# Kernel tuning notes

Hardware: AMD Instinct MI355X
Metric: run time of the kernel (lower is better)

The kernel has to match this reference:

```python
import jax, jax.numpy as jnp
import numpy as np

N_NODES = 100000
N_EDGES = 1600000
IN_CH, HID, OUT_CH = 512, 16, 64


def setup_inputs() -> dict:
    key = jax.random.key(0)
    ks = jax.random.split(key, 9)
    x = jax.random.normal(ks[0], (N_NODES, IN_CH), dtype=jnp.float32)
    edge_index1 = jax.random.randint(ks[1], (2, N_EDGES), 0, N_NODES, dtype=jnp.int32)
    edge_weight1 = jax.random.uniform(ks[2], (N_EDGES,), dtype=jnp.float32)
    edge_index2 = jax.random.randint(ks[3], (2, N_EDGES), 0, N_NODES, dtype=jnp.int32)
    edge_weight2 = jax.random.uniform(ks[4], (N_EDGES,), dtype=jnp.float32)
    W1 = jax.random.normal(ks[5], (IN_CH, HID), dtype=jnp.float32) / np.sqrt(IN_CH)
    b1 = jnp.zeros((HID,), dtype=jnp.float32)
    W2 = jax.random.normal(ks[6], (HID, OUT_CH), dtype=jnp.float32) / np.sqrt(HID)
    b2 = jnp.zeros((OUT_CH,), dtype=jnp.float32)
    return dict(x=x, edge_index1=edge_index1, edge_weight1=edge_weight1,
                edge_index2=edge_index2, edge_weight2=edge_weight2,
                W1=W1, b1=b1, W2=W2, b2=b2, num_nodes=N_NODES)


def _gcn_conv(x, W, b, row, col, w, num_nodes):
    # symmetric-normalized GCN aggregation: out = D^-1/2 A D^-1/2 (x W) + b
    deg = jax.ops.segment_sum(w, row, num_segments=num_nodes)  # [N]
    dinv = jnp.where(deg > 0, jax.lax.rsqrt(jnp.maximum(deg, 1e-12)), 0.0)
    norm = dinv[row] * w * dinv[col]                            # [E]
    h = x @ W                                                   # [N, F_out]
    msg = norm[:, None] * h[col]                                # [E, F_out]
    return jax.ops.segment_sum(msg, row, num_segments=num_nodes) + b


def reference(x, edge_index1, edge_weight1, edge_index2, edge_weight2,
              W1, b1, W2, b2, num_nodes):
    # concat edge lists; torch_sparse.coalesce(op='add') merges duplicates by
    # summing weights — the subsequent degree + scatter-add aggregation is
    # invariant to that dedup, so we run directly on the concatenated list.
    ei = jnp.concatenate([edge_index1, edge_index2], axis=1)    # [2, 2E]
    ew = jnp.concatenate([edge_weight1, edge_weight2])          # [2E]
    row, col = ei[0], ei[1]
    h = _gcn_conv(x, W1, b1, row, col, ew, num_nodes)
    h = jax.nn.relu(h)  # dropout is identity in eval mode
    h = _gcn_conv(h, W2, b2, row, col, ew, num_nodes)
    return jax.nn.log_softmax(h, axis=1)
```

## Files before the change

kernel.cpp:

```cpp
#include <hip/hip_runtime.h>
#include <hip/hip_bf16.h>

#define IN_CH 512
#define HID 16
#define OUT_CH 64
#define CAP 20480

typedef __attribute__((ext_vector_type(8))) short bf16x8;
typedef __attribute__((ext_vector_type(4))) float f32x4;

__device__ inline unsigned short f2bf(float f) {
    unsigned int u = __float_as_uint(f);
    return (unsigned short)((u + 0x7fffu + ((u >> 16) & 1u)) >> 16);
}

union A8 { bf16x8 v; short2 p[4]; };
__device__ inline short2 pk2(float a, float b) {
    union { __hip_bfloat162 h; short2 s; } u;
    u.h = __float22bfloat162_rn(make_float2(a, b));
    return u.s;
}

__global__ void k_init(int* __restrict__ cursors, int nbk) {
    int i = threadIdx.x;
    if (i < nbk) cursors[i] = i * CAP;
}

__global__ __launch_bounds__(1024) void k_partition(const int* __restrict__ ei1, const float* __restrict__ w1, int E1,
                                                    const int* __restrict__ ei2, const float* __restrict__ w2, int E2,
                                                    int* __restrict__ cursors,
                                                    uint2* __restrict__ packed, int Et) {
    __shared__ int hist[256];
    __shared__ int cur[256];
    int tid = threadIdx.x;
    if (tid < 256) hist[tid] = 0;
    __syncthreads();
    int e0 = blockIdx.x * 16384 + tid;
    #pragma unroll
    for (int j = 0; j < 16; ++j) {
        int e = e0 + j * 1024;
        if (e < Et) {
            int r = (e < E1) ? ei1[e] : ei2[e - E1];
            atomicAdd(&hist[r >> 9], 1);
        }
    }
    __syncthreads();
    if (tid < 256) {
        int h = hist[tid];
        cur[tid] = (h > 0) ? atomicAdd(&cursors[tid], h) : 0;
    }
    __syncthreads();
    #pragma unroll
    for (int j = 0; j < 16; ++j) {
        int e = e0 + j * 1024;
        if (e < Et) {
            int r, c; float w;
            if (e < E1) { r = ei1[e]; c = ei1[e + E1]; w = w1[e]; }
            else        { int f = e - E1; r = ei2[f]; c = ei2[f + E2]; w = w2[f]; }
            int b = r >> 9;
            int pos = atomicAdd(&cur[b], 1);
            packed[pos] = make_uint2(((unsigned)(r & 511) << 17) | (unsigned)c,
                                     __float_as_uint(w));
        }
    }
}

__global__ void k_bucket_scan(const int* __restrict__ cursors, int* __restrict__ cbase, int nbk) {
    __shared__ int s[256];
    int tid = threadIdx.x;
    int v = (tid < nbk) ? (cursors[tid] - tid * CAP) : 0;
    s[tid] = v;
    __syncthreads();
    for (int off = 1; off < 256; off <<= 1) {
        int t = (tid >= off) ? s[tid - off] : 0;
        __syncthreads();
        s[tid] += t;
        __syncthreads();
    }
    if (tid < nbk) cbase[tid] = s[tid] - v;
}

__global__ __launch_bounds__(1024) void k_buildcsr(const uint2* __restrict__ packed,
                                                   const int* __restrict__ cursors,
                                                   const int* __restrict__ cbase,
                                                   int* __restrict__ rowstart, int* __restrict__ cnt,
                                                   float* __restrict__ dinv, int2* __restrict__ csr, int N) {
    __shared__ int lcnt[512];
    __shared__ int lcur[512];
    __shared__ int lscan[512];
    __shared__ float ldeg[512];
    int b = blockIdx.x, tid = threadIdx.x;
    int M = cursors[b] - b * CAP;
    const uint2* pk = packed + (size_t)b * CAP;
    if (tid < 512) { lcnt[tid] = 0; ldeg[tid] = 0.f; }
    __syncthreads();
    for (int i = tid; i < M; i += 1024) atomicAdd(&lcnt[pk[i].x >> 17], 1);
    __syncthreads();
    int v = (tid < 512) ? lcnt[tid] : 0;
    if (tid < 512) lscan[tid] = v;
    __syncthreads();
    for (int off = 1; off < 512; off <<= 1) {
        int t = (tid >= off && tid < 512) ? lscan[tid - off] : 0;
        __syncthreads();
        if (tid < 512) lscan[tid] += t;
        __syncthreads();
    }
    int cb = cbase[b];
    if (tid < 512) {
        int ex = lscan[tid] - v;
        lcur[tid] = cb + ex;
        int node = b * 512 + tid;
        if (node < N) { rowstart[node] = cb + ex; cnt[node] = v; }
    }
    __syncthreads();
    for (int i = tid; i < M; i += 1024) {
        uint2 u = pk[i];
        int lr = u.x >> 17;
        int c  = u.x & 0x1FFFF;
        int p = atomicAdd(&lcur[lr], 1);
        csr[p] = make_int2(c, (int)u.y);
        atomicAdd(&ldeg[lr], __uint_as_float(u.y));
    }
    __syncthreads();
    if (tid < 512) {
        int node = b * 512 + tid;
        if (node < N) {
            float d = ldeg[tid];
            dinv[node] = (d > 0.f) ? rsqrtf(fmaxf(d, 1e-12f)) : 0.f;
        }
    }
}

__global__ void k_prep(const float* __restrict__ W1, unsigned short* __restrict__ W1s) {
    for (int p = threadIdx.x; p < 1024; p += 256) {
        int kc = p >> 6, lane = p & 63;
        int q = lane >> 4, m = lane & 15;
        int k0 = kc * 32 + q * 8;
        unsigned v[8];
        #pragma unroll
        for (int j = 0; j < 8; ++j) v[j] = f2bf(W1[(k0 + j) * HID + m]);
        uint4 o;
        o.x = v[0] | (v[1] << 16); o.y = v[2] | (v[3] << 16);
        o.z = v[4] | (v[5] << 16); o.w = v[6] | (v[7] << 16);
        ((uint4*)W1s)[p] = o;
    }
}

__global__ __launch_bounds__(256) void k_gemm1(const float* __restrict__ x,
                                               const unsigned short* __restrict__ W1s,
                                               const float* __restrict__ dinv,
                                               float* __restrict__ h1s, int n) {
    int wave = threadIdx.x >> 6, lane = threadIdx.x & 63;
    int tiles = (n + 15) >> 4;
    int t = blockIdx.x * 4 + wave;
    if (t >= tiles) return;

    int m = lane & 15, quad = lane >> 4;

    const bf16x8* Wv = (const bf16x8*)W1s;
    bf16x8 Bf[16];
    #pragma unroll
    for (int kc = 0; kc < 16; ++kc) Bf[kc] = Wv[kc * 64 + lane];

    int row = t * 16 + m;
    int rl = min(row, n - 1);
    const float4* xr = (const float4*)(x + (size_t)rl * IN_CH + quad * 8);

    f32x4 acc = {0.f, 0.f, 0.f, 0.f};
    #pragma unroll
    for (int kc = 0; kc < 16; ++kc) {
        float4 v0 = xr[kc * 8];
        float4 v1 = xr[kc * 8 + 1];
        A8 a;
        a.p[0] = pk2(v0.x, v0.y); a.p[1] = pk2(v0.z, v0.w);
        a.p[2] = pk2(v1.x, v1.y); a.p[3] = pk2(v1.z, v1.w);
        acc = __builtin_amdgcn_mfma_f32_16x16x32_bf16(a.v, Bf[kc], acc, 0, 0, 0);
    }

    int base = t * 16 + quad * 4;
    #pragma unroll
    for (int r = 0; r < 4; ++r) {
        int orow = base + r;
        if (orow < n) h1s[(size_t)orow * HID + m] = dinv[orow] * acc[r];
    }
}

__global__ __launch_bounds__(256) void k_agg1(const float* __restrict__ h1s,
                                              const int2* __restrict__ csr,
                                              const int* __restrict__ rowstart,
                                              const int* __restrict__ cnt,
                                              const float* __restrict__ dinv,
                                              const float* __restrict__ b1,
                                              float* __restrict__ out1s, int n) {
    int wave = threadIdx.x >> 6, lane = threadIdx.x & 63;
    int node = blockIdx.x * 4 + wave;
    if (node >= n) return;
    int slot = lane >> 2, c4 = lane & 3;
    const int2* ce = csr + rowstart[node];
    int deg = cnt[node];
    f32x4 acc = {0.f, 0.f, 0.f, 0.f};
    for (int i = slot; i < deg; i += 16) {
        int2 e = ce[i];
        float w = __int_as_float(e.y);
        float4 hv = ((const float4*)(h1s + (size_t)e.x * HID))[c4];
        acc[0] = fmaf(w, hv.x, acc[0]); acc[1] = fmaf(w, hv.y, acc[1]);
        acc[2] = fmaf(w, hv.z, acc[2]); acc[3] = fmaf(w, hv.w, acc[3]);
    }
    #pragma unroll
    for (int off = 4; off < 64; off <<= 1) {
        acc[0] += __shfl_xor(acc[0], off, 64);
        acc[1] += __shfl_xor(acc[1], off, 64);
        acc[2] += __shfl_xor(acc[2], off, 64);
        acc[3] += __shfl_xor(acc[3], off, 64);
    }
    if (lane < 4) {
        float dv = dinv[node];
        float4 bb = ((const float4*)b1)[c4];
        float4 o;
        o.x = fmaxf(fmaf(dv, acc[0], bb.x), 0.f) * dv;
        o.y = fmaxf(fmaf(dv, acc[1], bb.y), 0.f) * dv;
        o.z = fmaxf(fmaf(dv, acc[2], bb.z), 0.f) * dv;
        o.w = fmaxf(fmaf(dv, acc[3], bb.w), 0.f) * dv;
        ((float4*)(out1s + (size_t)node * HID))[c4] = o;
    }
}

__global__ __launch_bounds__(256) void k_layer2(const float* __restrict__ out1s,
                                                const int2* __restrict__ csr,
                                                const int* __restrict__ rowstart,
                                                const int* __restrict__ cnt,
                                                const float* __restrict__ dinv,
                                                const float* __restrict__ W2,
                                                const float* __restrict__ b2,
                                                float* __restrict__ out, int n) {
    __shared__ float W2l[HID * OUT_CH];
    for (int i = threadIdx.x; i < HID * OUT_CH; i += 256) W2l[i] = W2[i];
    __syncthreads();

    int wave = threadIdx.x >> 6, lane = threadIdx.x & 63;
    int node = blockIdx.x * 4 + wave;
    if (node >= n) return;
    int slot = lane >> 2, c4 = lane & 3;
    const int2* ce = csr + rowstart[node];
    int deg = cnt[node];
    f32x4 acc = {0.f, 0.f, 0.f, 0.f};
    for (int i = slot; i < deg; i += 16) {
        int2 e = ce[i];
        float w = __int_as_float(e.y);
        float4 hv = ((const float4*)(out1s + (size_t)e.x * HID))[c4];
        acc[0] = fmaf(w, hv.x, acc[0]); acc[1] = fmaf(w, hv.y, acc[1]);
        acc[2] = fmaf(w, hv.z, acc[2]); acc[3] = fmaf(w, hv.w, acc[3]);
    }
    #pragma unroll
    for (int off = 4; off < 64; off <<= 1) {
        acc[0] += __shfl_xor(acc[0], off, 64);
        acc[1] += __shfl_xor(acc[1], off, 64);
        acc[2] += __shfl_xor(acc[2], off, 64);
        acc[3] += __shfl_xor(acc[3], off, 64);
    }
    float dv = dinv[node];
    acc[0] *= dv; acc[1] *= dv; acc[2] *= dv; acc[3] *= dv;
    float v = b2[lane];
    #pragma unroll
    for (int gg = 0; gg < 4; ++gg) {
        float a0 = __shfl(acc[0], gg, 64);
        float a1 = __shfl(acc[1], gg, 64);
        float a2 = __shfl(acc[2], gg, 64);
        float a3 = __shfl(acc[3], gg, 64);
        v = fmaf(a0, W2l[(4 * gg + 0) * OUT_CH + lane], v);
        v = fmaf(a1, W2l[(4 * gg + 1) * OUT_CH + lane], v);
        v = fmaf(a2, W2l[(4 * gg + 2) * OUT_CH + lane], v);
        v = fmaf(a3, W2l[(4 * gg + 3) * OUT_CH + lane], v);
    }
    float m = v;
    #pragma unroll
    for (int off = 32; off; off >>= 1) m = fmaxf(m, __shfl_xor(m, off, 64));
    float ex = __expf(v - m);
    float s = ex;
    #pragma unroll
    for (int off = 32; off; off >>= 1) s += __shfl_xor(s, off, 64);
    out[(size_t)node * OUT_CH + lane] = (v - m) - __logf(s);
}

extern "C" void kernel_launch(void* const* d_in, const int* in_sizes, int n_in,
                              void* d_out, int out_size, void* d_ws, size_t ws_size,
                              hipStream_t stream) {
    const float* x   = (const float*)d_in[0];
    const int*   ei1 = (const int*)d_in[1];
    const float* w1  = (const float*)d_in[2];
    const int*   ei2 = (const int*)d_in[3];
    const float* w2  = (const float*)d_in[4];
    const float* W1  = (const float*)d_in[5];
    const float* b1  = (const float*)d_in[6];
    const float* W2  = (const float*)d_in[7];
    const float* b2  = (const float*)d_in[8];
    int N  = in_sizes[0] / IN_CH;
    int E1 = in_sizes[2];
    int E2 = in_sizes[4];
    int Et = E1 + E2;
    float* out = (float*)d_out;
    int nbk = (N + 511) >> 9;

    char* p = (char*)d_ws;
    int*   cursors  = (int*)p;   p += 1024;
    int*   cbase    = (int*)p;   p += 1024;
    int*   rowstart = (int*)p;   p += (size_t)N * 4;
    int*   cnt      = (int*)p;   p += (size_t)N * 4;
    float* dinv     = (float*)p; p += (size_t)N * 4;
    unsigned short* W1s = (unsigned short*)p; p += IN_CH * HID * 2;
    int2*  csr      = (int2*)p;  p += (size_t)Et * 8;
    uint2* packed   = (uint2*)p;
    float* h1s      = (float*)p;
    float* out1s    = h1s + (size_t)N * HID;

    k_init<<<1, 256, 0, stream>>>(cursors, nbk);
    k_prep<<<1, 256, 0, stream>>>(W1, W1s);
    k_partition<<<(Et + 16383) / 16384, 1024, 0, stream>>>(ei1, w1, E1, ei2, w2, E2,
                                                           cursors, packed, Et);
    k_bucket_scan<<<1, 256, 0, stream>>>(cursors, cbase, nbk);
    k_buildcsr<<<nbk, 1024, 0, stream>>>(packed, cursors, cbase,
                                         rowstart, cnt, dinv, csr, N);
    int tiles = (N + 15) / 16;
    k_gemm1<<<(tiles + 3) / 4, 256, 0, stream>>>(x, W1s, dinv, h1s, N);
    k_agg1<<<(N + 3) / 4, 256, 0, stream>>>(h1s, csr, rowstart, cnt, dinv, b1, out1s, N);
    k_layer2<<<(N + 3) / 4, 256, 0, stream>>>(out1s, csr, rowstart, cnt, dinv, W2, b2, out, N);
}
```

Measured before the change: 541.4 us.

## Replace CSR build with bucketed shared-memory atomic aggregation over partitioned edges

Drops the per-row CSR construction (bucket scan and CSR scatter) and instead aggregates directly from the 512-row bucketed edge list using shared-memory float atomics per bucket block. The partition kernel now stages edges locally in LDS so its global writes to each bucket are contiguous, and layer 2 computes each node's projection and log-softmax with two threads per node. This removes a full edge pass and its scattered writes. In exchange only about 196 blocks run per aggregation kernel, LDS atomics may contend, and summation order becomes nondeterministic.

```diff
diff --git a/kernel.cpp b/kernel.cpp
--- a/kernel.cpp
+++ b/kernel.cpp
@@ -5,6 +5,7 @@
 #define HID 16
 #define OUT_CH 64
 #define CAP 20480
+#define PE 8192
 
 typedef __attribute__((ext_vector_type(8))) short bf16x8;
 typedef __attribute__((ext_vector_type(4))) float f32x4;
@@ -31,95 +32,76 @@
                                                     int* __restrict__ cursors,
                                                     uint2* __restrict__ packed, int Et) {
     __shared__ int hist[256];
-    __shared__ int cur[256];
+    __shared__ int sc[256];
+    __shared__ int lbase[256];
+    __shared__ int gbase[256];
+    __shared__ int lcur[256];
+    __shared__ uint2 stage[PE];
+    __shared__ unsigned char bkt[PE];
     int tid = threadIdx.x;
+    int e0 = blockIdx.x * PE;
     if (tid < 256) hist[tid] = 0;
     __syncthreads();
-    int e0 = blockIdx.x * 16384 + tid;
-    #pragma unroll
-    for (int j = 0; j < 16; ++j) {
-        int e = e0 + j * 1024;
-        if (e < Et) {
-            int r = (e < E1) ? ei1[e] : ei2[e - E1];
-            atomicAdd(&hist[r >> 9], 1);
-        }
-    }
-    __syncthreads();
+    int r[8];
+    #pragma unroll
+    for (int j = 0; j < 8; ++j) {
+        int e = e0 + j * 1024 + tid;
+        int rr = -1;
+        if (e < Et) rr = (e < E1) ? ei1[e] : ei2[e - E1];
+        r[j] = rr;
+        if (rr >= 0) atomicAdd(&hist[rr >> 9], 1);
+    }
+    __syncthreads();
+    int v = (tid < 256) ? hist[tid] : 0;
+    if (tid < 256) sc[tid] = v;
+    __syncthreads();
+    for (int off = 1; off < 256; off <<= 1) {
+        int t = (tid >= off && tid < 256) ? sc[tid - off] : 0;
+        __syncthreads();
+        if (tid < 256) sc[tid] += t;
+        __syncthreads();
+    }
     if (tid < 256) {
-        int h = hist[tid];
-        cur[tid] = (h > 0) ? atomicAdd(&cursors[tid], h) : 0;
-    }
-    __syncthreads();
-    #pragma unroll
-    for (int j = 0; j < 16; ++j) {
-        int e = e0 + j * 1024;
-        if (e < Et) {
-            int r, c; float w;
-            if (e < E1) { r = ei1[e]; c = ei1[e + E1]; w = w1[e]; }
-            else        { int f = e - E1; r = ei2[f]; c = ei2[f + E2]; w = w2[f]; }
-            int b = r >> 9;
-            int pos = atomicAdd(&cur[b], 1);
-            packed[pos] = make_uint2(((unsigned)(r & 511) << 17) | (unsigned)c,
-                                     __float_as_uint(w));
-        }
-    }
-}
-
-__global__ void k_bucket_scan(const int* __restrict__ cursors, int* __restrict__ cbase, int nbk) {
-    __shared__ int s[256];
-    int tid = threadIdx.x;
-    int v = (tid < nbk) ? (cursors[tid] - tid * CAP) : 0;
-    s[tid] = v;
-    __syncthreads();
-    for (int off = 1; off < 256; off <<= 1) {
-        int t = (tid >= off) ? s[tid - off] : 0;
-        __syncthreads();
-        s[tid] += t;
-        __syncthreads();
-    }
-    if (tid < nbk) cbase[tid] = s[tid] - v;
-}
-
-__global__ __launch_bounds__(1024) void k_buildcsr(const uint2* __restrict__ packed,
-                                                   const int* __restrict__ cursors,
-                                                   const int* __restrict__ cbase,
-                                                   int* __restrict__ rowstart, int* __restrict__ cnt,
-                                                   float* __restrict__ dinv, int2* __restrict__ csr, int N) {
-    __shared__ int lcnt[512];
-    __shared__ int lcur[512];
-    __shared__ int lscan[512];
+        int ex = sc[tid] - v;
+        lbase[tid] = ex;
+        lcur[tid] = ex;
+        gbase[tid] = (v > 0) ? atomicAdd(&cursors[tid], v) : 0;
+    }
+    __syncthreads();
+    #pragma unroll
+    for (int j = 0; j < 8; ++j) {
+        if (r[j] >= 0) {
+            int e = e0 + j * 1024 + tid;
+            int cc; float ww;
+            if (e < E1) { cc = ei1[e + E1]; ww = w1[e]; }
+            else        { int f = e - E1; cc = ei2[f + E2]; ww = w2[f]; }
+            int bk = r[j] >> 9;
+            int pos = atomicAdd(&lcur[bk], 1);
+            stage[pos] = make_uint2(((unsigned)(r[j] & 511) << 17) | (unsigned)cc,
+                                    __float_as_uint(ww));
+            bkt[pos] = (unsigned char)bk;
+        }
+    }
+    __syncthreads();
+    int nv = min(PE, Et - e0);
+    for (int i = tid; i < nv; i += 1024) {
+        int bk = bkt[i];
+        packed[(size_t)gbase[bk] + (i - lbase[bk])] = stage[i];
+    }
+}
+
+__global__ __launch_bounds__(1024) void k_deg(const uint2* __restrict__ packed,
+                                              const int* __restrict__ cursors,
+                                              float* __restrict__ dinv, int N) {
     __shared__ float ldeg[512];
     int b = blockIdx.x, tid = threadIdx.x;
+    if (tid < 512) ldeg[tid] = 0.f;
+    __syncthreads();
     int M = cursors[b] - b * CAP;
     const uint2* pk = packed + (size_t)b * CAP;
-    if (tid < 512) { lcnt[tid] = 0; ldeg[tid] = 0.f; }
-    __syncthreads();
-    for (int i = tid; i < M; i += 1024) atomicAdd(&lcnt[pk[i].x >> 17], 1);
-    __syncthreads();
-    int v = (tid < 512) ? lcnt[tid] : 0;
-    if (tid < 512) lscan[tid] = v;
-    __syncthreads();
-    for (int off = 1; off < 512; off <<= 1) {
-        int t = (tid >= off && tid < 512) ? lscan[tid - off] : 0;
-        __syncthreads();
-        if (tid < 512) lscan[tid] += t;
-        __syncthreads();
-    }
-    int cb = cbase[b];
-    if (tid < 512) {
-        int ex = lscan[tid] - v;
-        lcur[tid] = cb + ex;
-        int node = b * 512 + tid;
-        if (node < N) { rowstart[node] = cb + ex; cnt[node] = v; }
-    }
-    __syncthreads();
     for (int i = tid; i < M; i += 1024) {
         uint2 u = pk[i];
-        int lr = u.x >> 17;
-        int c  = u.x & 0x1FFFF;
-        int p = atomicAdd(&lcur[lr], 1);
-        csr[p] = make_int2(c, (int)u.y);
-        atomicAdd(&ldeg[lr], __uint_as_float(u.y));
+        atomicAdd(&ldeg[u.x >> 17], __uint_as_float(u.y));
     }
     __syncthreads();
     if (tid < 512) {
@@ -185,101 +167,118 @@
     }
 }
 
-__global__ __launch_bounds__(256) void k_agg1(const float* __restrict__ h1s,
-                                              const int2* __restrict__ csr,
-                                              const int* __restrict__ rowstart,
-                                              const int* __restrict__ cnt,
-                                              const float* __restrict__ dinv,
-                                              const float* __restrict__ b1,
-                                              float* __restrict__ out1s, int n) {
-    int wave = threadIdx.x >> 6, lane = threadIdx.x & 63;
-    int node = blockIdx.x * 4 + wave;
-    if (node >= n) return;
-    int slot = lane >> 2, c4 = lane & 3;
-    const int2* ce = csr + rowstart[node];
-    int deg = cnt[node];
-    f32x4 acc = {0.f, 0.f, 0.f, 0.f};
-    for (int i = slot; i < deg; i += 16) {
-        int2 e = ce[i];
-        float w = __int_as_float(e.y);
-        float4 hv = ((const float4*)(h1s + (size_t)e.x * HID))[c4];
-        acc[0] = fmaf(w, hv.x, acc[0]); acc[1] = fmaf(w, hv.y, acc[1]);
-        acc[2] = fmaf(w, hv.z, acc[2]); acc[3] = fmaf(w, hv.w, acc[3]);
-    }
-    #pragma unroll
-    for (int off = 4; off < 64; off <<= 1) {
-        acc[0] += __shfl_xor(acc[0], off, 64);
-        acc[1] += __shfl_xor(acc[1], off, 64);
-        acc[2] += __shfl_xor(acc[2], off, 64);
-        acc[3] += __shfl_xor(acc[3], off, 64);
-    }
-    if (lane < 4) {
+__global__ __launch_bounds__(1024) void k_agg1(const float* __restrict__ h1s,
+                                               const uint2* __restrict__ packed,
+                                               const int* __restrict__ cursors,
+                                               const float* __restrict__ dinv,
+                                               const float* __restrict__ b1,
+                                               float* __restrict__ out1s, int N) {
+    __shared__ float accs[512 * 17];
+    int b = blockIdx.x, tid = threadIdx.x;
+    for (int i = tid; i < 512 * 17; i += 1024) accs[i] = 0.f;
+    __syncthreads();
+    int M = cursors[b] - b * CAP;
+    const uint2* pk = packed + (size_t)b * CAP;
+    int c4 = tid & 3;
+    for (int e = tid >> 2; e < M; e += 256) {
+        uint2 u = pk[e];
+        int lr = u.x >> 17;
+        int cc = u.x & 0x1FFFF;
+        float w = __uint_as_float(u.y);
+        float4 hv = ((const float4*)(h1s + (size_t)cc * HID))[c4];
+        int a0 = lr * 17 + c4 * 4;
+        atomicAdd(&accs[a0 + 0], w * hv.x);
+        atomicAdd(&accs[a0 + 1], w * hv.y);
+        atomicAdd(&accs[a0 + 2], w * hv.z);
+        atomicAdd(&accs[a0 + 3], w * hv.w);
+    }
+    __syncthreads();
+    if (tid < 512) {
+        int node = b * 512 + tid;
+        if (node < N) {
+            float dv = dinv[node];
+            float4* dst = (float4*)(out1s + (size_t)node * HID);
+            #pragma unroll
+            for (int q = 0; q < 4; ++q) {
+                float4 bb = ((const float4*)b1)[q];
+                float4 o;
+                o.x = fmaxf(fmaf(dv, accs[tid * 17 + q * 4 + 0], bb.x), 0.f) * dv;
+                o.y = fmaxf(fmaf(dv, accs[tid * 17 + q * 4 + 1], bb.y), 0.f) * dv;
+                o.z = fmaxf(fmaf(dv, accs[tid * 17 + q * 4 + 2], bb.z), 0.f) * dv;
+                o.w = fmaxf(fmaf(dv, accs[tid * 17 + q * 4 + 3], bb.w), 0.f) * dv;
+                dst[q] = o;
+            }
+        }
+    }
+}
+
+__global__ __launch_bounds__(1024) void k_layer2(const float* __restrict__ out1s,
+                                                 const uint2* __restrict__ packed,
+                                                 const int* __restrict__ cursors,
+                                                 const float* __restrict__ dinv,
+                                                 const float* __restrict__ W2,
+                                                 const float* __restrict__ b2,
+                                                 float* __restrict__ out, int N) {
+    __shared__ float accs[512 * 17];
+    __shared__ float W2l[HID * OUT_CH];
+    __shared__ float b2l[OUT_CH];
+    int b = blockIdx.x, tid = threadIdx.x;
+    for (int i = tid; i < 512 * 17; i += 1024) accs[i] = 0.f;
+    if (tid < HID * OUT_CH) W2l[tid] = W2[tid];
+    if (tid < OUT_CH) b2l[tid] = b2[tid];
+    __syncthreads();
+    int M = cursors[b] - b * CAP;
+    const uint2* pk = packed + (size_t)b * CAP;
+    int c4 = tid & 3;
+    for (int e = tid >> 2; e < M; e += 256) {
+        uint2 u = pk[e];
+        int lr = u.x >> 17;
+        int cc = u.x & 0x1FFFF;
+        float w = __uint_as_float(u.y);
+        float4 hv = ((const float4*)(out1s + (size_t)cc * HID))[c4];
+        int a0 = lr * 17 + c4 * 4;
+        atomicAdd(&accs[a0 + 0], w * hv.x);
+        atomicAdd(&accs[a0 + 1], w * hv.y);
+        atomicAdd(&accs[a0 + 2], w * hv.z);
+        atomicAdd(&accs[a0 + 3], w * hv.w);
+    }
+    __syncthreads();
+    int nd = tid >> 1, half = tid & 1, ch0 = half * 32;
+    int node = b * 512 + nd;
+    if (node < N) {
         float dv = dinv[node];
-        float4 bb = ((const float4*)b1)[c4];
-        float4 o;
-        o.x = fmaxf(fmaf(dv, acc[0], bb.x), 0.f) * dv;
-        o.y = fmaxf(fmaf(dv, acc[1], bb.y), 0.f) * dv;
-        o.z = fmaxf(fmaf(dv, acc[2], bb.z), 0.f) * dv;
-        o.w = fmaxf(fmaf(dv, acc[3], bb.w), 0.f) * dv;
-        ((float4*)(out1s + (size_t)node * HID))[c4] = o;
-    }
-}
-
-__global__ __launch_bounds__(256) void k_layer2(const float* __restrict__ out1s,
-                                                const int2* __restrict__ csr,
-                                                const int* __restrict__ rowstart,
-                                                const int* __restrict__ cnt,
-                                                const float* __restrict__ dinv,
-                                                const float* __restrict__ W2,
-                                                const float* __restrict__ b2,
-                                                float* __restrict__ out, int n) {
-    __shared__ float W2l[HID * OUT_CH];
-    for (int i = threadIdx.x; i < HID * OUT_CH; i += 256) W2l[i] = W2[i];
-    __syncthreads();
-
-    int wave = threadIdx.x >> 6, lane = threadIdx.x & 63;
-    int node = blockIdx.x * 4 + wave;
-    if (node >= n) return;
-    int slot = lane >> 2, c4 = lane & 3;
-    const int2* ce = csr + rowstart[node];
-    int deg = cnt[node];
-    f32x4 acc = {0.f, 0.f, 0.f, 0.f};
-    for (int i = slot; i < deg; i += 16) {
-        int2 e = ce[i];
-        float w = __int_as_float(e.y);
-        float4 hv = ((const float4*)(out1s + (size_t)e.x * HID))[c4];
-        acc[0] = fmaf(w, hv.x, acc[0]); acc[1] = fmaf(w, hv.y, acc[1]);
-        acc[2] = fmaf(w, hv.z, acc[2]); acc[3] = fmaf(w, hv.w, acc[3]);
-    }
-    #pragma unroll
-    for (int off = 4; off < 64; off <<= 1) {
-        acc[0] += __shfl_xor(acc[0], off, 64);
-        acc[1] += __shfl_xor(acc[1], off, 64);
-        acc[2] += __shfl_xor(acc[2], off, 64);
-        acc[3] += __shfl_xor(acc[3], off, 64);
-    }
-    float dv = dinv[node];
-    acc[0] *= dv; acc[1] *= dv; acc[2] *= dv; acc[3] *= dv;
-    float v = b2[lane];
-    #pragma unroll
-    for (int gg = 0; gg < 4; ++gg) {
-        float a0 = __shfl(acc[0], gg, 64);
-        float a1 = __shfl(acc[1], gg, 64);
-        float a2 = __shfl(acc[2], gg, 64);
-        float a3 = __shfl(acc[3], gg, 64);
-        v = fmaf(a0, W2l[(4 * gg + 0) * OUT_CH + lane], v);
-        v = fmaf(a1, W2l[(4 * gg + 1) * OUT_CH + lane], v);
-        v = fmaf(a2, W2l[(4 * gg + 2) * OUT_CH + lane], v);
-        v = fmaf(a3, W2l[(4 * gg + 3) * OUT_CH + lane], v);
-    }
-    float m = v;
-    #pragma unroll
-    for (int off = 32; off; off >>= 1) m = fmaxf(m, __shfl_xor(m, off, 64));
-    float ex = __expf(v - m);
-    float s = ex;
-    #pragma unroll
-    for (int off = 32; off; off >>= 1) s += __shfl_xor(s, off, 64);
-    out[(size_t)node * OUT_CH + lane] = (v - m) - __logf(s);
+        float a[16];
+        #pragma unroll
+        for (int k = 0; k < 16; ++k) a[k] = dv * accs[nd * 17 + k];
+        float vv[32];
+        #pragma unroll
+        for (int c = 0; c < 32; ++c) vv[c] = b2l[ch0 + c];
+        #pragma unroll
+        for (int k = 0; k < 16; ++k) {
+            #pragma unroll
+            for (int c = 0; c < 32; ++c)
+                vv[c] = fmaf(a[k], W2l[k * OUT_CH + ch0 + c], vv[c]);
+        }
+        float m = vv[0];
+        #pragma unroll
+        for (int c = 1; c < 32; ++c) m = fmaxf(m, vv[c]);
+        m = fmaxf(m, __shfl_xor(m, 1, 64));
+        float s = 0.f;
+        #pragma unroll
+        for (int c = 0; c < 32; ++c) s += __expf(vv[c] - m);
+        s += __shfl_xor(s, 1, 64);
+        float ls = __logf(s);
+        float4* dst = (float4*)(out + (size_t)node * OUT_CH + ch0);
+        #pragma unroll
+        for (int q = 0; q < 8; ++q) {
+            float4 o;
+            o.x = vv[q * 4 + 0] - m - ls;
+            o.y = vv[q * 4 + 1] - m - ls;
+            o.z = vv[q * 4 + 2] - m - ls;
+            o.w = vv[q * 4 + 3] - m - ls;
+            dst[q] = o;
+        }
+    }
 }
 
 extern "C" void kernel_launch(void* const* d_in, const int* in_sizes, int n_in,
@@ -303,25 +302,19 @@
 
     char* p = (char*)d_ws;
     int*   cursors  = (int*)p;   p += 1024;
-    int*   cbase    = (int*)p;   p += 1024;
-    int*   rowstart = (int*)p;   p += (size_t)N * 4;
-    int*   cnt      = (int*)p;   p += (size_t)N * 4;
     float* dinv     = (float*)p; p += (size_t)N * 4;
     unsigned short* W1s = (unsigned short*)p; p += IN_CH * HID * 2;
-    int2*  csr      = (int2*)p;  p += (size_t)Et * 8;
-    uint2* packed   = (uint2*)p;
-    float* h1s      = (float*)p;
-    float* out1s    = h1s + (size_t)N * HID;
+    uint2* packed   = (uint2*)p; p += (size_t)nbk * CAP * 8;
+    float* h1s      = (float*)p; p += (size_t)N * HID * 4;
+    float* out1s    = (float*)p;
 
     k_init<<<1, 256, 0, stream>>>(cursors, nbk);
     k_prep<<<1, 256, 0, stream>>>(W1, W1s);
-    k_partition<<<(Et + 16383) / 16384, 1024, 0, stream>>>(ei1, w1, E1, ei2, w2, E2,
-                                                           cursors, packed, Et);
-    k_bucket_scan<<<1, 256, 0, stream>>>(cursors, cbase, nbk);
-    k_buildcsr<<<nbk, 1024, 0, stream>>>(packed, cursors, cbase,
-                                         rowstart, cnt, dinv, csr, N);
+    k_partition<<<(Et + PE - 1) / PE, 1024, 0, stream>>>(ei1, w1, E1, ei2, w2, E2,
+                                                         cursors, packed, Et);
+    k_deg<<<nbk, 1024, 0, stream>>>(packed, cursors, dinv, N);
     int tiles = (N + 15) / 16;
     k_gemm1<<<(tiles + 3) / 4, 256, 0, stream>>>(x, W1s, dinv, h1s, N);
-    k_agg1<<<(N + 3) / 4, 256, 0, stream>>>(h1s, csr, rowstart, cnt, dinv, b1, out1s, N);
-    k_layer2<<<(N + 3) / 4, 256, 0, stream>>>(out1s, csr, rowstart, cnt, dinv, W2, b2, out, N);
-}
+    k_agg1<<<nbk, 1024, 0, stream>>>(h1s, packed, cursors, dinv, b1, out1s, N);
+    k_layer2<<<nbk, 1024, 0, stream>>>(out1s, packed, cursors, dinv, W2, b2, out, N);
+}
```

Result: slower. 1.065 ms (+96.7%).

## Stage partitioned edges in shared memory for coalesced bucket writes

Applied to the files above, without the earlier changes.

The partition kernel now scatters each block's edges into a shared-memory staging buffer ordered by bucket, using a local prefix scan over bucket counts. It then writes them out contiguously per bucket to global memory instead of issuing scattered 8-byte stores. The block size drops to 8192 edges and row indices are kept in registers rather than reloaded. This cuts uncoalesced global writes but adds a block-wide scan, about 72KB of LDS per block (lower occupancy), and twice as many global atomics on the bucket cursors.

```diff
diff --git a/kernel.cpp b/kernel.cpp
--- a/kernel.cpp
+++ b/kernel.cpp
@@ -5,6 +5,7 @@
 #define HID 16
 #define OUT_CH 64
 #define CAP 20480
+#define PE 8192
 
 typedef __attribute__((ext_vector_type(8))) short bf16x8;
 typedef __attribute__((ext_vector_type(4))) float f32x4;
@@ -31,37 +32,61 @@
                                                     int* __restrict__ cursors,
                                                     uint2* __restrict__ packed, int Et) {
     __shared__ int hist[256];
-    __shared__ int cur[256];
+    __shared__ int sc[256];
+    __shared__ int lbase[256];
+    __shared__ int gbase[256];
+    __shared__ int lcur[256];
+    __shared__ uint2 stage[PE];
+    __shared__ unsigned char bkt[PE];
     int tid = threadIdx.x;
+    int e0 = blockIdx.x * PE;
     if (tid < 256) hist[tid] = 0;
     __syncthreads();
-    int e0 = blockIdx.x * 16384 + tid;
-    #pragma unroll
-    for (int j = 0; j < 16; ++j) {
-        int e = e0 + j * 1024;
-        if (e < Et) {
-            int r = (e < E1) ? ei1[e] : ei2[e - E1];
-            atomicAdd(&hist[r >> 9], 1);
+    int r[8];
+    #pragma unroll
+    for (int j = 0; j < 8; ++j) {
+        int e = e0 + j * 1024 + tid;
+        int rr = -1;
+        if (e < Et) rr = (e < E1) ? ei1[e] : ei2[e - E1];
+        r[j] = rr;
+        if (rr >= 0) atomicAdd(&hist[rr >> 9], 1);
+    }
+    __syncthreads();
+    int v = (tid < 256) ? hist[tid] : 0;
+    if (tid < 256) sc[tid] = v;
+    __syncthreads();
+    for (int off = 1; off < 256; off <<= 1) {
+        int t = (tid >= off && tid < 256) ? sc[tid - off] : 0;
+        __syncthreads();
+        if (tid < 256) sc[tid] += t;
+        __syncthreads();
+    }
+    if (tid < 256) {
+        int ex = sc[tid] - v;
+        lbase[tid] = ex;
+        lcur[tid] = ex;
+        gbase[tid] = (v > 0) ? atomicAdd(&cursors[tid], v) : 0;
+    }
+    __syncthreads();
+    #pragma unroll
+    for (int j = 0; j < 8; ++j) {
+        if (r[j] >= 0) {
+            int e = e0 + j * 1024 + tid;
+            int cc; float ww;
+            if (e < E1) { cc = ei1[e + E1]; ww = w1[e]; }
+            else        { int f = e - E1; cc = ei2[f + E2]; ww = w2[f]; }
+            int bk = r[j] >> 9;
+            int pos = atomicAdd(&lcur[bk], 1);
+            stage[pos] = make_uint2(((unsigned)(r[j] & 511) << 17) | (unsigned)cc,
+                                    __float_as_uint(ww));
+            bkt[pos] = (unsigned char)bk;
         }
     }
     __syncthreads();
-    if (tid < 256) {
-        int h = hist[tid];
-        cur[tid] = (h > 0) ? atomicAdd(&cursors[tid], h) : 0;
-    }
-    __syncthreads();
-    #pragma unroll
-    for (int j = 0; j < 16; ++j) {
-        int e = e0 + j * 1024;
-        if (e < Et) {
-            int r, c; float w;
-            if (e < E1) { r = ei1[e]; c = ei1[e + E1]; w = w1[e]; }
-            else        { int f = e - E1; r = ei2[f]; c = ei2[f + E2]; w = w2[f]; }
-            int b = r >> 9;
-            int pos = atomicAdd(&cur[b], 1);
-            packed[pos] = make_uint2(((unsigned)(r & 511) << 17) | (unsigned)c,
-                                     __float_as_uint(w));
-        }
+    int nv = min(PE, Et - e0);
+    for (int i = tid; i < nv; i += 1024) {
+        int bk = bkt[i];
+        packed[(size_t)gbase[bk] + (i - lbase[bk])] = stage[i];
     }
 }
 
@@ -315,8 +340,8 @@
 
     k_init<<<1, 256, 0, stream>>>(cursors, nbk);
     k_prep<<<1, 256, 0, stream>>>(W1, W1s);
-    k_partition<<<(Et + 16383) / 16384, 1024, 0, stream>>>(ei1, w1, E1, ei2, w2, E2,
-                                                           cursors, packed, Et);
+    k_partition<<<(Et + PE - 1) / PE, 1024, 0, stream>>>(ei1, w1, E1, ei2, w2, E2,
+                                                         cursors, packed, Et);
     k_bucket_scan<<<1, 256, 0, stream>>>(cursors, cbase, nbk);
     k_buildcsr<<<nbk, 1024, 0, stream>>>(packed, cursors, cbase,
                                          rowstart, cnt, dinv, csr, N);
```

New measurement: 517.2 us. -4.5%, faster.
